# Optimization experiments

Hardware: AMD Instinct MI355X
Metric: run time of the kernel (lower is better)

Reference implementation:

```python
import jax, jax.numpy as jnp
import numpy as np

D = 1024      # hidden_size
FF = 4096     # ff_inner_dim = 4 * D
E = 8         # num_experts
K = 2         # moe_top_k
B, L = 4, 1024


def setup_inputs() -> dict:
    key = jax.random.key(0)
    ks = jax.random.split(key, 12)
    s = 0.02  # weight init scale
    return {
        "x": jax.random.normal(ks[0], (B, L, D), jnp.float32),
        "W_gate": jax.random.normal(ks[1], (D, E), jnp.float32) * s,
        "W1": jax.random.normal(ks[2], (E, D, FF), jnp.float32) * s,
        "b1": jnp.zeros((E, FF), jnp.float32),
        "W2": jax.random.normal(ks[3], (E, FF, D), jnp.float32) * s,
        "b2": jnp.zeros((E, D), jnp.float32),
        "Ws1": jax.random.normal(ks[4], (D, FF), jnp.float32) * s,
        "bs1": jnp.zeros((FF,), jnp.float32),
        "Ws2": jax.random.normal(ks[5], (FF, D), jnp.float32) * s,
        "bs2": jnp.zeros((D,), jnp.float32),
    }


def _gelu(h):
    # torch F.gelu default = exact (erf) gelu
    return jax.nn.gelu(h, approximate=False)


def reference(x, W_gate, W1, b1, W2, b2, Ws1, bs1, Ws2, bs2):
    Bx, Lx, Dx = x.shape
    xf = x.reshape(-1, Dx)                       # [T, D]
    logits = xf @ W_gate                         # [T, E]
    probs = jax.nn.softmax(logits, axis=-1)
    top_v, top_i = jax.lax.top_k(probs, K)       # [T, K]
    top_v = top_v / jnp.sum(top_v, axis=-1, keepdims=True)
    # dense combine weights: [T, E], zero for unselected experts
    combine = jnp.sum(jax.nn.one_hot(top_i, E, dtype=xf.dtype) * top_v[..., None], axis=1)

    out = jnp.zeros_like(xf)
    for e in range(E):  # fixed small expert loop, unrolled under jit
        h = _gelu(xf @ W1[e] + b1[e])            # [T, FF]
        out = out + combine[:, e:e + 1] * (h @ W2[e] + b2[e])

    shared = _gelu(xf @ Ws1 + bs1) @ Ws2 + bs2   # [T, D]
    return (out + shared).reshape(Bx, Lx, Dx)
```

## Files before the change

### kernel.cpp

```cpp
#include <hip/hip_runtime.h>
#include <hip/hip_bf16.h>

typedef unsigned short ushort_t;
typedef __attribute__((ext_vector_type(4))) float f32x4;
typedef __attribute__((ext_vector_type(8))) short bf16x8;
typedef __attribute__((ext_vector_type(8))) unsigned short us8;

#define T_TOK 4096
#define D_DIM 1024
#define FF_DIM 4096
#define NE 8
#define ESTRIDE 4194304L

__device__ __forceinline__ unsigned short f2bf(float f) {
  __hip_bfloat16 h = __float2bfloat16(f);
  return __builtin_bit_cast(unsigned short, h);
}
__device__ __forceinline__ float gelu_f(float v) {
  return 0.5f * v * (1.0f + erff(v * 0.70710678118654752440f));
}

__global__ __launch_bounds__(256) void pre_kernel(
    const float* __restrict__ x, const float* __restrict__ Wg,
    const float* __restrict__ W1, const float* __restrict__ Ws1,
    int* __restrict__ cnt, int* __restrict__ tok,
    float* __restrict__ wof, int* __restrict__ rankof,
    ushort_t* __restrict__ Xbf, ushort_t* __restrict__ W1T) {
  __shared__ ushort_t tile[128][136];
  const int bid = blockIdx.x, tid = threadIdx.x;

  if (bid < 1024) {
    const int t = bid * 4 + (tid >> 6);
    const int lane = tid & 63;
    const float* xr = x + (long)t * D_DIM;
    ushort_t* xb = Xbf + (long)t * D_DIM;
    float acc[NE];
#pragma unroll
    for (int e = 0; e < NE; e++) acc[e] = 0.f;
#pragma unroll
    for (int i = 0; i < 16; i++) {
      int d = i * 64 + lane;
      float xv = xr[d];
      xb[d] = f2bf(xv);
      const float* wr = Wg + d * NE;
#pragma unroll
      for (int e = 0; e < NE; e++) acc[e] += xv * wr[e];
    }
#pragma unroll
    for (int off = 32; off > 0; off >>= 1) {
#pragma unroll
      for (int e = 0; e < NE; e++) acc[e] += __shfl_xor(acc[e], off, 64);
    }
    if (lane == 0) {
      int i0 = 0;
#pragma unroll
      for (int e = 1; e < NE; e++) if (acc[e] > acc[i0]) i0 = e;
      int i1 = -1;
#pragma unroll
      for (int e = 0; e < NE; e++) {
        if (e == i0) continue;
        if (i1 < 0 || acc[e] > acc[i1]) i1 = e;
      }
      float e1 = expf(acc[i1] - acc[i0]);
      float w0 = 1.f / (1.f + e1);
      float w1 = e1 * w0;
      int s0 = atomicAdd(&cnt[i0], 1);
      tok[i0 * T_TOK + s0] = t; wof[i0 * T_TOK + s0] = w0; rankof[i0 * T_TOK + s0] = 0;
      int s1 = atomicAdd(&cnt[i1], 1);
      tok[i1 * T_TOK + s1] = t; wof[i1 * T_TOK + s1] = w1; rankof[i1 * T_TOK + s1] = 1;
      tok[8 * T_TOK + t] = t; wof[8 * T_TOK + t] = 1.f; rankof[8 * T_TOK + t] = 0;
    }
    return;
  }

  int tix = bid - 1024;
  if (tix >= 2304) return;
  const int e = tix >> 8;
  const int rem = tix & 255;
  const int r0 = (rem >> 5) * 128, c0 = (rem & 31) * 128;
  const float* src = (e == 8) ? Ws1 : (W1 + (long)e * 4194304);
  ushort_t* d = W1T + (long)e * ESTRIDE;
#pragma unroll
  for (int i = 0; i < 16; i++) {
    int lin = tid + i * 256;
    int r = lin >> 5, c = (lin & 31) * 4;
    float4 v = *(const float4*)(src + (long)(r0 + r) * 4096 + c0 + c);
    tile[c + 0][r] = f2bf(v.x);
    tile[c + 1][r] = f2bf(v.y);
    tile[c + 2][r] = f2bf(v.z);
    tile[c + 3][r] = f2bf(v.w);
  }
  __syncthreads();
#pragma unroll
  for (int i = 0; i < 8; i++) {
    int lin = tid + i * 256;
    int cc = lin >> 4, rp = lin & 15;
    us8 v = *(const us8*)&tile[cc][rp * 8];
    *(us8*)(d + (long)(c0 + cc) * 1024 + r0 + rp * 8) = v;
  }
}

__global__ void build_queue_kernel(const int* __restrict__ cnt, int* __restrict__ base,
                                   unsigned int* __restrict__ q1,
                                   unsigned int* __restrict__ q2,
                                   int* __restrict__ nq, int* __restrict__ cnt8) {
  const int e = blockIdx.x;
  int off1 = 0, off2 = 0, tot1 = 0, tot2 = 0, M = 0;
  for (int i = 0; i < 9; i++) {
    int c = (i == 8) ? T_TOK : cnt[i];
    int m = (c + 255) >> 8;
    if (i < e) { off1 += m * 16; off2 += m * 4; }
    if (i == e) M = m;
    tot1 += m * 16; tot2 += m * 4;
  }
  for (int i = threadIdx.x; i < M * 16; i += 256) {
    int my = i >> 4, nx = i & 15;
    int ms = my >> 1, mi = my & 1, ns = nx >> 2, ni = nx & 3;
    int h = M - ms * 2; if (h > 2) h = 2;
    int pos = ms * 32 + ns * (h * 4) + mi * 4 + ni;
    q1[off1 + pos] = ((unsigned)e << 16) | ((unsigned)my << 8) | (unsigned)nx;
  }
  for (int i = threadIdx.x; i < M * 4; i += 256) {
    int my = i >> 2, nx = i & 3;
    int pos = nx * M + my;
    q2[off2 + pos] = ((unsigned)e << 16) | ((unsigned)my << 8) | (unsigned)nx;
  }
  if (e == 0 && threadIdx.x == 0) {
    nq[0] = tot1; nq[1] = tot2;
    int s = 0;
    for (int i = 0; i < NE; i++) { base[i] = s; s += cnt[i]; }
    base[8] = s;
    *cnt8 = T_TOK;
  }
}

template <int K, int N, int PHASE, bool FUSE>
__global__ __launch_bounds__(1024, 1) void gemm_kernel(
    const ushort_t* __restrict__ Abase, const ushort_t* __restrict__ WT,
    const float* __restrict__ bias_e, const float* __restrict__ bias_s,
    const int* __restrict__ cnt, const int* __restrict__ base,
    const int* __restrict__ tok, const float* __restrict__ wof,
    const int* __restrict__ rankof,
    const unsigned int* __restrict__ q, const int* __restrict__ nq_all,
    ushort_t* __restrict__ He, float* __restrict__ ybuf, float* __restrict__ out,
    const float* __restrict__ W2src, const float* __restrict__ Ws2src,
    ushort_t* __restrict__ W2Tdst) {
  __shared__ char smem[65536];
  const int tid = threadIdx.x;
  const int bid = blockIdx.x;
  const int NBLK = FUSE ? 1024 : (int)gridDim.x;

  if (FUSE && bid >= 1024) {
    int tix = bid - 1024;
    if (tix >= 2304) return;
    const int e = tix >> 8;
    const int rem = tix & 255;
    const int r0 = (rem >> 3) * 128, c0 = (rem & 7) * 128;
    const float* src = (e == 8) ? Ws2src : (W2src + (long)e * 4194304);
    ushort_t* d = W2Tdst + (long)e * ESTRIDE;
    ushort_t (*tile)[136] = (ushort_t (*)[136])smem;
#pragma unroll
    for (int i = 0; i < 4; i++) {
      int lin = tid + i * 1024;
      int r = lin >> 5, c = (lin & 31) * 4;
      float4 v = *(const float4*)(src + (long)(r0 + r) * 1024 + c0 + c);
      tile[c + 0][r] = f2bf(v.x);
      tile[c + 1][r] = f2bf(v.y);
      tile[c + 2][r] = f2bf(v.z);
      tile[c + 3][r] = f2bf(v.w);
    }
    __syncthreads();
#pragma unroll
    for (int i = 0; i < 2; i++) {
      int lin = tid + i * 1024;
      int cc = lin >> 4, rp = lin & 15;
      us8 v = *(const us8*)&tile[cc][rp * 8];
      *(us8*)(d + (long)(c0 + cc) * 4096 + r0 + rp * 8) = v;
    }
    return;
  }

  const int nq = nq_all[PHASE - 1];
  const int chunk = NBLK >> 3;
  const int vbid = (bid < (chunk << 3)) ? ((bid & 7) * chunk + (bid >> 3)) : bid;

  const int w = tid >> 6, lane = tid & 63;
  const int wm = w >> 2, wn = w & 3;
  const int lr = lane & 15, lg = lane >> 4;
  char* const lds = smem;

  const int srow = tid >> 2;
  const int cg = ((tid & 3) - (srow >> 1)) & 3;

  int offA[4], offB[4];
#pragma unroll
  for (int m = 0; m < 4; m++) {
    int r = wm * 64 + m * 16 + lr;
    offA[m] = r * 64 + (((lg + (r >> 1)) & 3) << 4);
  }
#pragma unroll
  for (int n = 0; n < 4; n++) {
    int r = wn * 64 + n * 16 + lr;
    offB[n] = r * 64 + (((lg + (r >> 1)) & 3) << 4);
  }

  constexpr int NT = K / 32;

#define STAGE(buf_, kk_)                                                        \
  do {                                                                          \
    char* dd_ = lds + (buf_) * 32768 + tid * 16;                                \
    __builtin_amdgcn_global_load_lds(                                           \
        (const __attribute__((address_space(1))) void*)(pA + (kk_)),            \
        (__attribute__((address_space(3))) void*)(dd_), 16, 0, 0);              \
    __builtin_amdgcn_global_load_lds(                                           \
        (const __attribute__((address_space(1))) void*)(pB + (kk_)),            \
        (__attribute__((address_space(3))) void*)(dd_ + 16384), 16, 0, 0);      \
  } while (0)

  for (int it = vbid; it < nq; it += NBLK) {
    const unsigned int item = q[it];
    const int e = item >> 16;
    const int m0 = ((item >> 8) & 0xff) * 256;
    const int n0 = (item & 0xff) * 256;
    const int count = cnt[e];

    int rr = m0 + srow;
    int rc = (rr < count) ? rr : 0;
    long arow;
    if (PHASE == 1) arow = tok[e * T_TOK + rc];
    else            arow = (long)base[e] + rc;
    const ushort_t* pA = Abase + arow * (long)K + cg * 8;
    const ushort_t* pB = WT + (long)e * ESTRIDE + (long)(n0 + srow) * K + cg * 8;

    f32x4 acc[4][4] = {};

    __builtin_amdgcn_s_barrier();
    asm volatile("" ::: "memory");
    STAGE(0, 0);

    for (int t = 0; t < NT; t++) {
      if (t + 1 < NT) {
        STAGE((t + 1) & 1, (t + 1) * 32);
        asm volatile("s_waitcnt vmcnt(2)" ::: "memory");
      } else {
        asm volatile("s_waitcnt vmcnt(0)" ::: "memory");
      }
      __builtin_amdgcn_s_barrier();
      asm volatile("" ::: "memory");

      const char* aB = lds + (t & 1) * 32768;
      const char* bB = aB + 16384;
      bf16x8 av[4], bv[4];
#pragma unroll
      for (int m = 0; m < 4; m++) av[m] = *(const bf16x8*)(aB + offA[m]);
#pragma unroll
      for (int n = 0; n < 4; n++) bv[n] = *(const bf16x8*)(bB + offB[n]);
#pragma unroll
      for (int m = 0; m < 4; m++)
#pragma unroll
        for (int n = 0; n < 4; n++)
          acc[m][n] = __builtin_amdgcn_mfma_f32_16x16x32_bf16(av[m], bv[n], acc[m][n], 0, 0, 0);

      __builtin_amdgcn_s_barrier();
      asm volatile("" ::: "memory");
    }

    const float* bias = (e == NE) ? bias_s : (bias_e + (long)e * N);
#pragma unroll
    for (int m = 0; m < 4; m++) {
#pragma unroll
      for (int j = 0; j < 4; j++) {
        int rloc = wm * 64 + m * 16 + lg * 4 + j;
        int rrr = m0 + rloc;
        if (rrr >= count) continue;
        if (PHASE == 1) {
          long orow = (long)base[e] + rrr;
#pragma unroll
          for (int n = 0; n < 4; n++) {
            int col = n0 + wn * 64 + n * 16 + lr;
            float v = acc[m][n][j] + bias[col];
            He[orow * FF_DIM + col] = f2bf(gelu_f(v));
          }
        } else {
          int tt = tok[e * T_TOK + rrr];
          if (e == NE) {
#pragma unroll
            for (int n = 0; n < 4; n++) {
              int col = n0 + wn * 64 + n * 16 + lr;
              out[(long)tt * D_DIM + col] = acc[m][n][j] + bias[col];
            }
          } else {
            float wgt = wof[e * T_TOK + rrr];
            int rk = rankof[e * T_TOK + rrr];
            float* dst = ybuf + (long)rk * ((long)T_TOK * D_DIM) + (long)tt * D_DIM;
#pragma unroll
            for (int n = 0; n < 4; n++) {
              int col = n0 + wn * 64 + n * 16 + lr;
              dst[col] = wgt * (acc[m][n][j] + bias[col]);
            }
          }
        }
      }
    }
  }
#undef STAGE
}

__global__ void final_add_kernel(float* __restrict__ out, const float* __restrict__ ybuf) {
  long i = ((long)blockIdx.x * 256 + threadIdx.x) * 4;
  float4 a = *(const float4*)(out + i);
  float4 b = *(const float4*)(ybuf + i);
  float4 c = *(const float4*)(ybuf + (long)T_TOK * D_DIM + i);
  a.x += b.x + c.x; a.y += b.y + c.y; a.z += b.z + c.z; a.w += b.w + c.w;
  *(float4*)(out + i) = a;
}

extern "C" void kernel_launch(void* const* d_in, const int* in_sizes, int n_in,
                              void* d_out, int out_size, void* d_ws, size_t ws_size,
                              hipStream_t stream) {
  (void)in_sizes; (void)n_in; (void)out_size; (void)ws_size;
  const float* x   = (const float*)d_in[0];
  const float* Wg  = (const float*)d_in[1];
  const float* W1  = (const float*)d_in[2];
  const float* b1  = (const float*)d_in[3];
  const float* W2  = (const float*)d_in[4];
  const float* b2  = (const float*)d_in[5];
  const float* Ws1 = (const float*)d_in[6];
  const float* bs1 = (const float*)d_in[7];
  const float* Ws2 = (const float*)d_in[8];
  const float* bs2 = (const float*)d_in[9];
  float* out = (float*)d_out;

  char* ws = (char*)d_ws;
  int*      cnt    = (int*)(ws + 0);
  int*      base   = (int*)(ws + 64);
  int*      tok    = (int*)(ws + 256);
  float*    wof    = (float*)(ws + 256 + 147456);
  int*      rankof = (int*)(ws + 256 + 2 * 147456);
  ushort_t* Xbf    = (ushort_t*)(ws + 442624);
  ushort_t* W1T    = (ushort_t*)(ws + 8831232);
  ushort_t* W2T    = (ushort_t*)(ws + 84328704);
  ushort_t* He     = (ushort_t*)(ws + 159826176);
  int*      nq     = (int*)(ws + 260489472);
  unsigned int* q1 = (unsigned int*)(ws + 260489536);
  unsigned int* q2 = (unsigned int*)(ws + 260489536 + 32768);
  float*    ybuf   = (float*)(ws + 261538048);

  hipMemsetAsync(cnt, 0, 64, stream);
  pre_kernel<<<3328, 256, 0, stream>>>(x, Wg, W1, Ws1, cnt, tok, wof, rankof, Xbf, W1T);
  build_queue_kernel<<<9, 256, 0, stream>>>(cnt, base, q1, q2, nq, &cnt[8]);
  gemm_kernel<1024, 4096, 1, true><<<3328, 1024, 0, stream>>>(
      Xbf, W1T, b1, bs1, cnt, base, tok, wof, rankof, q1, nq, He, ybuf, out,
      W2, Ws2, W2T);
  gemm_kernel<4096, 1024, 2, false><<<256, 1024, 0, stream>>>(
      He, W2T, b2, bs2, cnt, base, tok, wof, rankof, q2, nq, He, ybuf, out,
      nullptr, nullptr, nullptr);
  final_add_kernel<<<4096, 256, 0, stream>>>(out, ybuf);
}
```

Measured before the change: 507.7 us.

## Shrink GEMM tiles to 128x256 with 512 threads and split-K phase 2

Switches both grouped GEMMs from 256x256 tiles and 1024-thread blocks to 128x256 tiles with 512 threads, less LDS and launch bounds allowing several blocks per CU. The queue is rebuilt for the finer M granularity, and the fused W2 transpose path is adjusted to the new block size. Phase 2 splits K in half across two work items that accumulate with atomicAdd into zero-initialised outputs, which adds memsets and atomic traffic. The aim is more parallelism and better load balance for the small down-projection grid, at the cost of less reuse per tile and atomic contention.

```diff
diff --git a/kernel.cpp b/kernel.cpp
--- a/kernel.cpp
+++ b/kernel.cpp
@@ -108,16 +108,16 @@
   int off1 = 0, off2 = 0, tot1 = 0, tot2 = 0, M = 0;
   for (int i = 0; i < 9; i++) {
     int c = (i == 8) ? T_TOK : cnt[i];
-    int m = (c + 255) >> 8;
+    int m = (c + 127) >> 7;
     if (i < e) { off1 += m * 16; off2 += m * 4; }
     if (i == e) M = m;
     tot1 += m * 16; tot2 += m * 4;
   }
   for (int i = threadIdx.x; i < M * 16; i += 256) {
     int my = i >> 4, nx = i & 15;
-    int ms = my >> 1, mi = my & 1, ns = nx >> 2, ni = nx & 3;
-    int h = M - ms * 2; if (h > 2) h = 2;
-    int pos = ms * 32 + ns * (h * 4) + mi * 4 + ni;
+    int ms = my >> 2, mi = my & 3, ns = nx >> 2, ni = nx & 3;
+    int h = M - ms * 4; if (h > 4) h = 4;
+    int pos = ms * 64 + ns * (h * 4) + mi * 4 + ni;
     q1[off1 + pos] = ((unsigned)e << 16) | ((unsigned)my << 8) | (unsigned)nx;
   }
   for (int i = threadIdx.x; i < M * 4; i += 256) {
@@ -135,7 +135,7 @@
 }
 
 template <int K, int N, int PHASE, bool FUSE>
-__global__ __launch_bounds__(1024, 1) void gemm_kernel(
+__global__ __launch_bounds__(512, 4) void gemm_kernel(
     const ushort_t* __restrict__ Abase, const ushort_t* __restrict__ WT,
     const float* __restrict__ bias_e, const float* __restrict__ bias_s,
     const int* __restrict__ cnt, const int* __restrict__ base,
@@ -145,13 +145,13 @@
     ushort_t* __restrict__ He, float* __restrict__ ybuf, float* __restrict__ out,
     const float* __restrict__ W2src, const float* __restrict__ Ws2src,
     ushort_t* __restrict__ W2Tdst) {
-  __shared__ char smem[65536];
+  __shared__ char smem[49152];
   const int tid = threadIdx.x;
   const int bid = blockIdx.x;
-  const int NBLK = FUSE ? 1024 : (int)gridDim.x;
-
-  if (FUSE && bid >= 1024) {
-    int tix = bid - 1024;
+  const int NBLK = FUSE ? 1792 : (int)gridDim.x;
+
+  if (FUSE && bid >= 1792) {
+    int tix = bid - 1792;
     if (tix >= 2304) return;
     const int e = tix >> 8;
     const int rem = tix & 255;
@@ -160,8 +160,8 @@
     ushort_t* d = W2Tdst + (long)e * ESTRIDE;
     ushort_t (*tile)[136] = (ushort_t (*)[136])smem;
 #pragma unroll
-    for (int i = 0; i < 4; i++) {
-      int lin = tid + i * 1024;
+    for (int i = 0; i < 8; i++) {
+      int lin = tid + i * 512;
       int r = lin >> 5, c = (lin & 31) * 4;
       float4 v = *(const float4*)(src + (long)(r0 + r) * 1024 + c0 + c);
       tile[c + 0][r] = f2bf(v.x);
@@ -171,8 +171,8 @@
     }
     __syncthreads();
 #pragma unroll
-    for (int i = 0; i < 2; i++) {
-      int lin = tid + i * 1024;
+    for (int i = 0; i < 4; i++) {
+      int lin = tid + i * 512;
       int cc = lin >> 4, rp = lin & 15;
       us8 v = *(const us8*)&tile[cc][rp * 8];
       *(us8*)(d + (long)(c0 + cc) * 4096 + r0 + rp * 8) = v;
@@ -181,6 +181,7 @@
   }
 
   const int nq = nq_all[PHASE - 1];
+  const int nwork = (PHASE == 2) ? nq * 2 : nq;
   const int chunk = NBLK >> 3;
   const int vbid = (bid < (chunk << 3)) ? ((bid & 7) * chunk + (bid >> 3)) : bid;
 
@@ -201,36 +202,44 @@
 #pragma unroll
   for (int n = 0; n < 4; n++) {
     int r = wn * 64 + n * 16 + lr;
-    offB[n] = r * 64 + (((lg + (r >> 1)) & 3) << 4);
-  }
-
-  constexpr int NT = K / 32;
+    offB[n] = 8192 + r * 64 + (((lg + (r >> 1)) & 3) << 4);
+  }
+
+  constexpr int KS = (PHASE == 2) ? K / 2 : K;
+  constexpr int NT = KS / 32;
 
 #define STAGE(buf_, kk_)                                                        \
   do {                                                                          \
-    char* dd_ = lds + (buf_) * 32768 + tid * 16;                                \
+    char* dd_ = lds + (buf_) * 24576 + tid * 16;                                \
     __builtin_amdgcn_global_load_lds(                                           \
         (const __attribute__((address_space(1))) void*)(pA + (kk_)),            \
         (__attribute__((address_space(3))) void*)(dd_), 16, 0, 0);              \
     __builtin_amdgcn_global_load_lds(                                           \
-        (const __attribute__((address_space(1))) void*)(pB + (kk_)),            \
+        (const __attribute__((address_space(1))) void*)(pB0 + (kk_)),           \
+        (__attribute__((address_space(3))) void*)(dd_ + 8192), 16, 0, 0);       \
+    __builtin_amdgcn_global_load_lds(                                           \
+        (const __attribute__((address_space(1))) void*)(pB1 + (kk_)),           \
         (__attribute__((address_space(3))) void*)(dd_ + 16384), 16, 0, 0);      \
   } while (0)
 
-  for (int it = vbid; it < nq; it += NBLK) {
+  for (int iw = vbid; iw < nwork; iw += NBLK) {
+    const int it = (PHASE == 2) ? (iw >> 1) : iw;
+    const int ks = (PHASE == 2) ? (iw & 1) : 0;
     const unsigned int item = q[it];
     const int e = item >> 16;
-    const int m0 = ((item >> 8) & 0xff) * 256;
+    const int m0 = ((item >> 8) & 0xff) * 128;
     const int n0 = (item & 0xff) * 256;
     const int count = cnt[e];
+    const long kofs = (long)ks * KS;
 
     int rr = m0 + srow;
     int rc = (rr < count) ? rr : 0;
     long arow;
     if (PHASE == 1) arow = tok[e * T_TOK + rc];
     else            arow = (long)base[e] + rc;
-    const ushort_t* pA = Abase + arow * (long)K + cg * 8;
-    const ushort_t* pB = WT + (long)e * ESTRIDE + (long)(n0 + srow) * K + cg * 8;
+    const ushort_t* pA  = Abase + arow * (long)K + kofs + cg * 8;
+    const ushort_t* pB0 = WT + (long)e * ESTRIDE + (long)(n0 + srow) * K + kofs + cg * 8;
+    const ushort_t* pB1 = pB0 + 128L * K;
 
     f32x4 acc[4][4] = {};
 
@@ -241,18 +250,17 @@
     for (int t = 0; t < NT; t++) {
       if (t + 1 < NT) {
         STAGE((t + 1) & 1, (t + 1) * 32);
-        asm volatile("s_waitcnt vmcnt(2)" ::: "memory");
+        asm volatile("s_waitcnt vmcnt(3)" ::: "memory");
       } else {
         asm volatile("s_waitcnt vmcnt(0)" ::: "memory");
       }
       __builtin_amdgcn_s_barrier();
       asm volatile("" ::: "memory");
 
-      const char* aB = lds + (t & 1) * 32768;
-      const char* bB = aB + 16384;
+      const char* bB = lds + (t & 1) * 24576;
       bf16x8 av[4], bv[4];
 #pragma unroll
-      for (int m = 0; m < 4; m++) av[m] = *(const bf16x8*)(aB + offA[m]);
+      for (int m = 0; m < 4; m++) av[m] = *(const bf16x8*)(bB + offA[m]);
 #pragma unroll
       for (int n = 0; n < 4; n++) bv[n] = *(const bf16x8*)(bB + offB[n]);
 #pragma unroll
@@ -287,7 +295,8 @@
 #pragma unroll
             for (int n = 0; n < 4; n++) {
               int col = n0 + wn * 64 + n * 16 + lr;
-              out[(long)tt * D_DIM + col] = acc[m][n][j] + bias[col];
+              float v = acc[m][n][j] + (ks == 0 ? bias[col] : 0.f);
+              atomicAdd(&out[(long)tt * D_DIM + col], v);
             }
           } else {
             float wgt = wof[e * T_TOK + rrr];
@@ -296,7 +305,8 @@
 #pragma unroll
             for (int n = 0; n < 4; n++) {
               int col = n0 + wn * 64 + n * 16 + lr;
-              dst[col] = wgt * (acc[m][n][j] + bias[col]);
+              float v = acc[m][n][j] + (ks == 0 ? bias[col] : 0.f);
+              atomicAdd(&dst[col], wgt * v);
             }
           }
         }
@@ -347,12 +357,14 @@
   float*    ybuf   = (float*)(ws + 261538048);
 
   hipMemsetAsync(cnt, 0, 64, stream);
+  hipMemsetAsync(ybuf, 0, 2L * T_TOK * D_DIM * 4, stream);
+  hipMemsetAsync(out, 0, (long)T_TOK * D_DIM * 4, stream);
   pre_kernel<<<3328, 256, 0, stream>>>(x, Wg, W1, Ws1, cnt, tok, wof, rankof, Xbf, W1T);
   build_queue_kernel<<<9, 256, 0, stream>>>(cnt, base, q1, q2, nq, &cnt[8]);
-  gemm_kernel<1024, 4096, 1, true><<<3328, 1024, 0, stream>>>(
+  gemm_kernel<1024, 4096, 1, true><<<4096, 512, 0, stream>>>(
       Xbf, W1T, b1, bs1, cnt, base, tok, wof, rankof, q1, nq, He, ybuf, out,
       W2, Ws2, W2T);
-  gemm_kernel<4096, 1024, 2, false><<<256, 1024, 0, stream>>>(
+  gemm_kernel<4096, 1024, 2, false><<<768, 512, 0, stream>>>(
       He, W2T, b2, bs2, cnt, base, tok, wof, rankof, q2, nq, He, ybuf, out,
       nullptr, nullptr, nullptr);
   final_add_kernel<<<4096, 256, 0, stream>>>(out, ybuf);
```

Result: slower. 596.7 us (+17.5%).
